# Optimization experiments

Measured on AMD Instinct MI355X. Metric: run time of the kernel, lower is better.

The kernel has to match this reference:

```python
import jax, jax.numpy as jnp
import numpy as np

BATCH_SIZE = 8192   # args.batch_size
NUM_VIEWS = 2       # args.num_views
TEMPERATURE = 0.07  # args.loss_args['temperature']
FEAT_DIM = 256
N = (BATCH_SIZE // 2) * NUM_VIEWS  # rows of features


def _static_index_maps():
    # labels = sorted cat of num_views copies of arange(batch_size//2)
    labels = np.sort(np.tile(np.arange(BATCH_SIZE // 2), NUM_VIEWS))
    lab_mat = labels[None, :] == labels[:, None]          # (N, N) bool
    # off-diagonal column indices: for row i, columns [0..N-1] excluding i,
    # in ascending order (matches torch boolean-mask extraction order)
    j = np.arange(N - 1)
    cols = j[None, :] + (j[None, :] >= np.arange(N)[:, None])  # (N, N-1)
    lab_off = np.take_along_axis(lab_mat, cols, axis=1)        # (N, N-1) bool
    k = NUM_VIEWS - 1  # positives per row
    # stable sort puts positive positions first, preserving column order
    order = np.argsort(~lab_off, axis=1, kind='stable')
    pos_cols = order[:, :k]   # (N, k)
    neg_cols = order[:, k:]   # (N, N-1-k)
    return cols, pos_cols, neg_cols

_COLS, _POS_COLS, _NEG_COLS = _static_index_maps()


def setup_inputs() -> dict:
    key = jax.random.key(0)
    features = jax.random.normal(key, (N, FEAT_DIM), dtype=jnp.float32)
    return {"features": features}


def reference(features):
    # L2 normalize rows (F.normalize eps clamp)
    norm = jnp.maximum(jnp.linalg.norm(features, axis=1, keepdims=True), 1e-12)
    f = features / norm
    sim = f @ f.T                                            # (N, N)
    sim_off = jnp.take_along_axis(sim, jnp.asarray(_COLS), axis=1)       # (N, N-1)
    positives = jnp.take_along_axis(sim_off, jnp.asarray(_POS_COLS), axis=1)
    negatives = jnp.take_along_axis(sim_off, jnp.asarray(_NEG_COLS), axis=1)
    logits = jnp.concatenate([positives, negatives], axis=1) / TEMPERATURE
    # CrossEntropyLoss with target class 0 for every row
    loss = jnp.mean(-jax.nn.log_softmax(logits, axis=1)[:, 0])
    return loss
```

## Files before the change

kernel.cpp:

```cpp
#include <hip/hip_runtime.h>
#include <stdint.h>

#define N_ROWS 8192
#define FEAT   256
#define RB     256
#define NB     (N_ROWS / RB)
#define NPAIR  (NB * (NB + 1) / 2)
#define NSLOT  (2 * NB)
#define CT     64

typedef __bf16 bf16x8 __attribute__((ext_vector_type(8)));
typedef float  f32x4  __attribute__((ext_vector_type(4)));

__device__ __forceinline__ unsigned short f2bf(float x) {
    union { float f; uint32_t u; } v; v.f = x;
    uint32_t u = v.u;
    return (unsigned short)((u + 0x7FFFu + ((u >> 16) & 1u)) >> 16);
}

__device__ __forceinline__ void gld16(const unsigned short* g, unsigned short* l) {
    __builtin_amdgcn_global_load_lds((__attribute__((address_space(1))) void*)g,
                                     (__attribute__((address_space(3))) void*)l,
                                     16, 0, 0);
}

__global__ void knorm(const float* __restrict__ feat,
                      unsigned short* __restrict__ fb,
                      float* __restrict__ pos) {
    __shared__ float ex[4][FEAT];
    int wave = threadIdx.x >> 6;
    int lane = threadIdx.x & 63;
    int row  = blockIdx.x * 4 + wave;
    float4 v = ((const float4*)(feat + row * FEAT))[lane];
    float ss = v.x*v.x + v.y*v.y + v.z*v.z + v.w*v.w;
    #pragma unroll
    for (int off = 1; off < 64; off <<= 1) ss += __shfl_xor(ss, off);
    float inv = 1.0f / fmaxf(sqrtf(ss), 1e-12f);
    float4 o; o.x = v.x*inv; o.y = v.y*inv; o.z = v.z*inv; o.w = v.w*inv;
    ushort4 b;
    b.x = f2bf(o.x); b.y = f2bf(o.y); b.z = f2bf(o.z); b.w = f2bf(o.w);
    int sidx = (((lane >> 1) ^ (row & 7)) << 1) | (lane & 1);
    ((ushort4*)(fb + row * FEAT))[sidx] = b;
    ((float4*)ex[wave])[lane] = o;
    __syncthreads();
    float4 p = ((float4*)ex[wave ^ 1])[lane];
    float d = o.x*p.x + o.y*p.y + o.z*p.z + o.w*p.w;
    #pragma unroll
    for (int off = 1; off < 64; off <<= 1) d += __shfl_xor(d, off);
    if (lane == 0) pos[row] = d;
}

__global__ __launch_bounds__(256, 1)
void kmain(const unsigned short* __restrict__ fb, float* __restrict__ partial) {
    __shared__ unsigned short bufA[CT * FEAT];
    __shared__ unsigned short bufB[CT * FEAT];
    __shared__ float colred[4][128];
    const int t    = threadIdx.x;
    const int lane = t & 63;
    const int wave = t >> 6;
    const int quad = lane >> 4;
    const int l15  = lane & 15;

    const int pair = blockIdx.x >> 1;
    const int h    = blockIdx.x & 1;
    int a = 0, rem = pair;
    while (rem >= NB - a) { rem -= NB - a; ++a; }
    const int b = a + rem;
    const bool isdiag = (a == b);

    const int rw    = a * RB + wave * 64;
    const int cbase = b * RB + h * 128;
    const float Kc = 20.60992915555662f;

#define STAGE(DST, CC0) do {                                                  \
    const unsigned short* sp_ = fb + (size_t)(cbase + (CC0)) * FEAT + t * 8;  \
    unsigned short* dp_ = (DST) + t * 8;                                      \
    _Pragma("unroll")                                                         \
    for (int i_ = 0; i_ < 8; ++i_)                                            \
        gld16(sp_ + i_ * 2048, dp_ + i_ * 2048);                              \
} while (0)

    STAGE(bufA, 0);

    bf16x8 af[4][8];
    #pragma unroll
    for (int rf = 0; rf < 4; ++rf)
        #pragma unroll
        for (int ks = 0; ks < 8; ++ks) {
            int row = rw + rf * 16 + l15;
            int ch  = (ks * 4 + quad) ^ (row & 7);
            af[rf][ks] = *(const bf16x8*)(fb + row * FEAT + ch * 8);
        }

    float lsum[4][4] = {{0.f,0.f,0.f,0.f},{0.f,0.f,0.f,0.f},
                        {0.f,0.f,0.f,0.f},{0.f,0.f,0.f,0.f}};
    float cs[8] = {0.f,0.f,0.f,0.f,0.f,0.f,0.f,0.f};

#define EPI(AC, RF, G) do {                                                   \
    const int rb_ = rw + (RF) * 16;                                           \
    const bool dg_ = (cg == rb_);        \
    _Pragma("unroll")                                                         \
    for (int r_ = 0; r_ < 4; ++r_) {                                          \
        float e_ = __builtin_amdgcn_exp2f(fmaf((AC)[r_], Kc, -Kc));           \
        if (dg_ && (rb_ + quad * 4 + r_ == C)) e_ = 0.f;     \
        lsum[(RF)][r_] += e_;                                                 \
        cs[(G)] += e_;                                                        \
    }                                                                         \
} while (0)

#define COMPUTE(BS, CC0, CS0) do {                                            \
    _Pragma("unroll")                                                         \
    for (int g = 0; g < 4; ++g) {                                             \
        const int cg = cbase + (CC0) + g * 16;                                \
        const int C  = cg + l15;                                              \
        f32x4 ac0 = {0.f,0.f,0.f,0.f};                                        \
        f32x4 ac1 = {0.f,0.f,0.f,0.f};                                        \
        f32x4 ac2 = {0.f,0.f,0.f,0.f};                                        \
        f32x4 ac3 = {0.f,0.f,0.f,0.f};                                        \
        _Pragma("unroll")                                                     \
        for (int ks = 0; ks < 8; ++ks) {                                      \
            bf16x8 bv = *(const bf16x8*)((BS) + (g * 16 + l15) * FEAT         \
                                        + (((ks * 4 + quad) ^ (l15 & 7)) * 8)); \
            ac0 = __builtin_amdgcn_mfma_f32_16x16x32_bf16(af[0][ks], bv, ac0, 0, 0, 0); \
            ac1 = __builtin_amdgcn_mfma_f32_16x16x32_bf16(af[1][ks], bv, ac1, 0, 0, 0); \
            ac2 = __builtin_amdgcn_mfma_f32_16x16x32_bf16(af[2][ks], bv, ac2, 0, 0, 0); \
            ac3 = __builtin_amdgcn_mfma_f32_16x16x32_bf16(af[3][ks], bv, ac3, 0, 0, 0); \
        }                                                                     \
        EPI(ac0, 0, (CS0) + g); EPI(ac1, 1, (CS0) + g);                       \
        EPI(ac2, 2, (CS0) + g); EPI(ac3, 3, (CS0) + g);                       \
    }                                                                         \
} while (0)

    asm volatile("s_waitcnt vmcnt(0)" ::: "memory");
    __builtin_amdgcn_s_barrier();
    STAGE(bufB, CT);
    COMPUTE(bufA, 0, 0);
    asm volatile("s_waitcnt vmcnt(0)" ::: "memory");
    __builtin_amdgcn_s_barrier();
    COMPUTE(bufB, CT, 4);

    const int rslot = 2 * b + h;
    #pragma unroll
    for (int rf = 0; rf < 4; ++rf)
        #pragma unroll
        for (int r = 0; r < 4; ++r) {
            float v = lsum[rf][r];
            v += __shfl_xor(v, 1);
            v += __shfl_xor(v, 2);
            v += __shfl_xor(v, 4);
            v += __shfl_xor(v, 8);
            lsum[rf][r] = v;
        }
    if (l15 == 0) {
        #pragma unroll
        for (int rf = 0; rf < 4; ++rf)
            #pragma unroll
            for (int r = 0; r < 4; ++r) {
                int row = rw + rf * 16 + quad * 4 + r;
                partial[rslot * N_ROWS + row] = lsum[rf][r];
            }
    }

    #pragma unroll
    for (int g = 0; g < 8; ++g) {
        float v = cs[g];
        v += __shfl_xor(v, 16);
        v += __shfl_xor(v, 32);
        if (lane < 16) colred[wave][g * 16 + l15] = v;
    }
    __syncthreads();
    if (!isdiag && t < 128) {
        float s = colred[0][t] + colred[1][t] + colred[2][t] + colred[3][t];
        partial[(2 * a) * N_ROWS + b * RB + h * 128 + t] = s;
    }
    if (isdiag && h == 0) {
        for (int j = 0; j < a; ++j)
            partial[(2 * j + 1) * N_ROWS + a * RB + t] = 0.f;
    }
#undef STAGE
#undef COMPUTE
#undef EPI
}

__global__ void kreduce(const float* __restrict__ partial,
                        const float* __restrict__ pos,
                        float* __restrict__ bsum) {
    __shared__ float red[4];
    int row  = blockIdx.x * 256 + threadIdx.x;
    int wave = threadIdx.x >> 6;
    int lane = threadIdx.x & 63;
    float L = 0.f;
    #pragma unroll
    for (int p = 0; p < NSLOT; ++p) L += partial[p * N_ROWS + row];
    const float invT = 14.285714285714286f;
    float loss = invT * (1.0f - pos[row])
               + 0.6931471805599453f * __builtin_amdgcn_logf(L);
    #pragma unroll
    for (int off = 1; off < 64; off <<= 1) loss += __shfl_xor(loss, off);
    if (lane == 0) red[wave] = loss;
    __syncthreads();
    if (threadIdx.x == 0)
        bsum[blockIdx.x] = red[0] + red[1] + red[2] + red[3];
}

__global__ void kfinal(const float* __restrict__ bsum, float* __restrict__ out) {
    int lane = threadIdx.x;
    float v = (lane < 32) ? bsum[lane] : 0.f;
    #pragma unroll
    for (int off = 1; off < 32; off <<= 1) v += __shfl_xor(v, off);
    if (lane == 0) out[0] = v * (1.0f / 8192.0f);
}

extern "C" void kernel_launch(void* const* d_in, const int* in_sizes, int n_in,
                              void* d_out, int out_size, void* d_ws, size_t ws_size,
                              hipStream_t stream) {
    const float* feat = (const float*)d_in[0];
    float* out = (float*)d_out;
    char* ws = (char*)d_ws;
    unsigned short* fb      = (unsigned short*)ws;
    float*          partial = (float*)(ws + (4u << 20));
    float*          pos     = (float*)(ws + (6u << 20));
    float*          bsum    = (float*)(ws + (6u << 20) + (1u << 15));

    knorm<<<N_ROWS / 4, 256, 0, stream>>>(feat, fb, pos);
    kmain<<<NPAIR * 2, 256, 0, stream>>>(fb, partial);
    kreduce<<<N_ROWS / 256, 256, 0, stream>>>(partial, pos, bsum);
    kfinal<<<1, 64, 0, stream>>>(bsum, out);
}
```

Before: 121.1 us.

## Shrink tiles to 128x128 with single LDS buffer for higher occupancy

Halves the row block size so each block computes a 128x128 tile with 2 row fragments per wave. It drops the double-buffered LDS staging for a single buffer and allows 4 blocks per CU. The symmetric partial-sum layout is simplified so every slot is written by exactly one block, which removes the zero-fill pass. The reduction kernel is restructured to split slots across waves. The intent is more concurrent waves to hide latency, traded against more redundant fragment loads and loss of intra-block copy/compute overlap.

```diff
diff --git a/kernel.cpp b/kernel.cpp
--- a/kernel.cpp
+++ b/kernel.cpp
@@ -3,10 +3,10 @@
 
 #define N_ROWS 8192
 #define FEAT   256
-#define RB     256
+#define RB     128
 #define NB     (N_ROWS / RB)
 #define NPAIR  (NB * (NB + 1) / 2)
-#define NSLOT  (2 * NB)
+#define NSLOT  NB
 #define CT     64
 
 typedef __bf16 bf16x8 __attribute__((ext_vector_type(8)));
@@ -50,41 +50,38 @@
     if (lane == 0) pos[row] = d;
 }
 
-__global__ __launch_bounds__(256, 1)
+__global__ __launch_bounds__(256, 4)
 void kmain(const unsigned short* __restrict__ fb, float* __restrict__ partial) {
-    __shared__ unsigned short bufA[CT * FEAT];
-    __shared__ unsigned short bufB[CT * FEAT];
-    __shared__ float colred[4][128];
+    __shared__ unsigned short buf[CT * FEAT];
+    __shared__ float colred[4][RB];
     const int t    = threadIdx.x;
     const int lane = t & 63;
     const int wave = t >> 6;
     const int quad = lane >> 4;
     const int l15  = lane & 15;
 
-    const int pair = blockIdx.x >> 1;
-    const int h    = blockIdx.x & 1;
-    int a = 0, rem = pair;
+    int a = 0, rem = blockIdx.x;
     while (rem >= NB - a) { rem -= NB - a; ++a; }
     const int b = a + rem;
     const bool isdiag = (a == b);
 
-    const int rw    = a * RB + wave * 64;
-    const int cbase = b * RB + h * 128;
+    const int rw    = a * RB + wave * 32;
+    const int cbase = b * RB;
     const float Kc = 20.60992915555662f;
 
-#define STAGE(DST, CC0) do {                                                  \
+#define STAGE(CC0) do {                                                       \
     const unsigned short* sp_ = fb + (size_t)(cbase + (CC0)) * FEAT + t * 8;  \
-    unsigned short* dp_ = (DST) + t * 8;                                      \
+    unsigned short* dp_ = buf + t * 8;                                        \
     _Pragma("unroll")                                                         \
     for (int i_ = 0; i_ < 8; ++i_)                                            \
         gld16(sp_ + i_ * 2048, dp_ + i_ * 2048);                              \
 } while (0)
 
-    STAGE(bufA, 0);
-
-    bf16x8 af[4][8];
-    #pragma unroll
-    for (int rf = 0; rf < 4; ++rf)
+    STAGE(0);
+
+    bf16x8 af[2][8];
+    #pragma unroll
+    for (int rf = 0; rf < 2; ++rf)
         #pragma unroll
         for (int ks = 0; ks < 8; ++ks) {
             int row = rw + rf * 16 + l15;
@@ -92,56 +89,50 @@
             af[rf][ks] = *(const bf16x8*)(fb + row * FEAT + ch * 8);
         }
 
-    float lsum[4][4] = {{0.f,0.f,0.f,0.f},{0.f,0.f,0.f,0.f},
-                        {0.f,0.f,0.f,0.f},{0.f,0.f,0.f,0.f}};
+    float lsum[2][4] = {{0.f,0.f,0.f,0.f},{0.f,0.f,0.f,0.f}};
     float cs[8] = {0.f,0.f,0.f,0.f,0.f,0.f,0.f,0.f};
 
-#define EPI(AC, RF, G) do {                                                   \
-    const int rb_ = rw + (RF) * 16;                                           \
-    const bool dg_ = (cg == rb_);        \
-    _Pragma("unroll")                                                         \
-    for (int r_ = 0; r_ < 4; ++r_) {                                          \
-        float e_ = __builtin_amdgcn_exp2f(fmaf((AC)[r_], Kc, -Kc));           \
-        if (dg_ && (rb_ + quad * 4 + r_ == C)) e_ = 0.f;     \
-        lsum[(RF)][r_] += e_;                                                 \
-        cs[(G)] += e_;                                                        \
-    }                                                                         \
-} while (0)
-
-#define COMPUTE(BS, CC0, CS0) do {                                            \
+#define COMPUTE(CC0, CS0) do {                                                \
     _Pragma("unroll")                                                         \
     for (int g = 0; g < 4; ++g) {                                             \
         const int cg = cbase + (CC0) + g * 16;                                \
         const int C  = cg + l15;                                              \
         f32x4 ac0 = {0.f,0.f,0.f,0.f};                                        \
         f32x4 ac1 = {0.f,0.f,0.f,0.f};                                        \
-        f32x4 ac2 = {0.f,0.f,0.f,0.f};                                        \
-        f32x4 ac3 = {0.f,0.f,0.f,0.f};                                        \
         _Pragma("unroll")                                                     \
         for (int ks = 0; ks < 8; ++ks) {                                      \
-            bf16x8 bv = *(const bf16x8*)((BS) + (g * 16 + l15) * FEAT         \
+            bf16x8 bv = *(const bf16x8*)(buf + (g * 16 + l15) * FEAT          \
                                         + (((ks * 4 + quad) ^ (l15 & 7)) * 8)); \
             ac0 = __builtin_amdgcn_mfma_f32_16x16x32_bf16(af[0][ks], bv, ac0, 0, 0, 0); \
             ac1 = __builtin_amdgcn_mfma_f32_16x16x32_bf16(af[1][ks], bv, ac1, 0, 0, 0); \
-            ac2 = __builtin_amdgcn_mfma_f32_16x16x32_bf16(af[2][ks], bv, ac2, 0, 0, 0); \
-            ac3 = __builtin_amdgcn_mfma_f32_16x16x32_bf16(af[3][ks], bv, ac3, 0, 0, 0); \
         }                                                                     \
-        EPI(ac0, 0, (CS0) + g); EPI(ac1, 1, (CS0) + g);                       \
-        EPI(ac2, 2, (CS0) + g); EPI(ac3, 3, (CS0) + g);                       \
+        _Pragma("unroll")                                                     \
+        for (int rf = 0; rf < 2; ++rf) {                                      \
+            const int rb_ = rw + rf * 16;                                     \
+            const bool dg_ = (cg == rb_);         \
+            const f32x4 ac = (rf == 0) ? ac0 : ac1;                           \
+            _Pragma("unroll")                                                 \
+            for (int r = 0; r < 4; ++r) {                                     \
+                float e = __builtin_amdgcn_exp2f(fmaf(ac[r], Kc, -Kc));       \
+                if (dg_ && (rb_ + quad * 4 + r == C)) e = 0.f;    \
+                lsum[rf][r] += e;                                             \
+                cs[(CS0) + g] += e;                                           \
+            }                                                                 \
+        }                                                                     \
     }                                                                         \
 } while (0)
 
     asm volatile("s_waitcnt vmcnt(0)" ::: "memory");
     __builtin_amdgcn_s_barrier();
-    STAGE(bufB, CT);
-    COMPUTE(bufA, 0, 0);
+    COMPUTE(0, 0);
+    __builtin_amdgcn_s_barrier();
+    STAGE(CT);
     asm volatile("s_waitcnt vmcnt(0)" ::: "memory");
     __builtin_amdgcn_s_barrier();
-    COMPUTE(bufB, CT, 4);
-
-    const int rslot = 2 * b + h;
-    #pragma unroll
-    for (int rf = 0; rf < 4; ++rf)
+    COMPUTE(CT, 4);
+
+    #pragma unroll
+    for (int rf = 0; rf < 2; ++rf)
         #pragma unroll
         for (int r = 0; r < 4; ++r) {
             float v = lsum[rf][r];
@@ -153,11 +144,11 @@
         }
     if (l15 == 0) {
         #pragma unroll
-        for (int rf = 0; rf < 4; ++rf)
+        for (int rf = 0; rf < 2; ++rf)
             #pragma unroll
             for (int r = 0; r < 4; ++r) {
                 int row = rw + rf * 16 + quad * 4 + r;
-                partial[rslot * N_ROWS + row] = lsum[rf][r];
+                partial[b * N_ROWS + row] = lsum[rf][r];
             }
     }
 
@@ -169,45 +160,42 @@
         if (lane < 16) colred[wave][g * 16 + l15] = v;
     }
     __syncthreads();
-    if (!isdiag && t < 128) {
+    if (!isdiag && t < RB) {
         float s = colred[0][t] + colred[1][t] + colred[2][t] + colred[3][t];
-        partial[(2 * a) * N_ROWS + b * RB + h * 128 + t] = s;
-    }
-    if (isdiag && h == 0) {
-        for (int j = 0; j < a; ++j)
-            partial[(2 * j + 1) * N_ROWS + a * RB + t] = 0.f;
-    }
-#undef STAGE
-#undef COMPUTE
-#undef EPI
+        partial[a * N_ROWS + b * RB + t] = s;
+    }
 }
 
 __global__ void kreduce(const float* __restrict__ partial,
                         const float* __restrict__ pos,
                         float* __restrict__ bsum) {
-    __shared__ float red[4];
-    int row  = blockIdx.x * 256 + threadIdx.x;
+    __shared__ float red[4][64];
     int wave = threadIdx.x >> 6;
     int lane = threadIdx.x & 63;
+    int row0 = blockIdx.x * 64;
     float L = 0.f;
     #pragma unroll
-    for (int p = 0; p < NSLOT; ++p) L += partial[p * N_ROWS + row];
-    const float invT = 14.285714285714286f;
-    float loss = invT * (1.0f - pos[row])
-               + 0.6931471805599453f * __builtin_amdgcn_logf(L);
-    #pragma unroll
-    for (int off = 1; off < 64; off <<= 1) loss += __shfl_xor(loss, off);
-    if (lane == 0) red[wave] = loss;
+    for (int p = 0; p < 16; ++p)
+        L += partial[(size_t)(wave * 16 + p) * N_ROWS + row0 + lane];
+    red[wave][lane] = L;
     __syncthreads();
-    if (threadIdx.x == 0)
-        bsum[blockIdx.x] = red[0] + red[1] + red[2] + red[3];
+    if (wave == 0) {
+        float Lt = red[0][lane] + red[1][lane] + red[2][lane] + red[3][lane];
+        int row = row0 + lane;
+        const float invT = 14.285714285714286f;
+        float loss = invT * (1.0f - pos[row])
+                   + 0.6931471805599453f * __builtin_amdgcn_logf(Lt);
+        #pragma unroll
+        for (int off = 1; off < 64; off <<= 1) loss += __shfl_xor(loss, off);
+        if (lane == 0) bsum[blockIdx.x] = loss;
+    }
 }
 
 __global__ void kfinal(const float* __restrict__ bsum, float* __restrict__ out) {
     int lane = threadIdx.x;
-    float v = (lane < 32) ? bsum[lane] : 0.f;
-    #pragma unroll
-    for (int off = 1; off < 32; off <<= 1) v += __shfl_xor(v, off);
+    float v = bsum[lane] + bsum[lane + 64];
+    #pragma unroll
+    for (int off = 1; off < 64; off <<= 1) v += __shfl_xor(v, off);
     if (lane == 0) out[0] = v * (1.0f / 8192.0f);
 }
 
@@ -223,7 +211,7 @@
     float*          bsum    = (float*)(ws + (6u << 20) + (1u << 15));
 
     knorm<<<N_ROWS / 4, 256, 0, stream>>>(feat, fb, pos);
-    kmain<<<NPAIR * 2, 256, 0, stream>>>(fb, partial);
-    kreduce<<<N_ROWS / 256, 256, 0, stream>>>(partial, pos, bsum);
+    kmain<<<NPAIR, 256, 0, stream>>>(fb, partial);
+    kreduce<<<N_ROWS / 64, 256, 0, stream>>>(partial, pos, bsum);
     kfinal<<<1, 64, 0, stream>>>(bsum, out);
 }
```

Measured after the change: 99.40 us (median of 2 runs). 1.22x faster.
